# Kernel tuning notes

Measured on AMD Instinct MI355X. Metric: run time of the kernel, lower is better.

## Reference

```python
import jax, jax.numpy as jnp
import numpy as np
from jax import lax

N_SAMPLES1 = 128   # self.n_samples[0]
K = 64             # k in sample_and_group
RADIUS = 0.4       # self.radius[0]
BN_EPS = 1e-5
NEG_INF = -1e8
DIMS0 = [6, 64, 64, 128]      # mlps_in[0][0] -> mlps[0]
DIMS1 = [131, 128, 128, 512]  # 128+3 -> mlps[1] (use_light_weight=False)


def _fps(pos, n):
    # pos: (N,3) -> (n,) indices; deterministic start at point 0
    Np = pos.shape[0]
    def body(carry, _):
        dists, last = carry
        d = jnp.sum((pos - pos[last]) ** 2, axis=-1)
        dists = jnp.minimum(dists, d)
        return (dists, jnp.argmax(dists).astype(jnp.int32)), last
    _, idxs = lax.scan(body, (jnp.full((Np,), 1e10, pos.dtype), jnp.int32(0)), None, length=n)
    return idxs


def _gather(values, idx):
    # values (B,N,C), idx (B,...) -> (B,...,C)
    return jax.vmap(lambda v, i: v[i])(values, idx)


def _conv_bn_relu(x, W, b, g, be):
    # 1x1 Conv2d + BatchNorm2d (training-mode batch stats) + ReLU; x (B,n,k,Cin)
    y = jnp.einsum('bnkc,cd->bnkd', x, W) + b
    m = jnp.mean(y, axis=(0, 1, 2), keepdims=True)
    v = jnp.mean(jnp.square(y - m), axis=(0, 1, 2), keepdims=True)
    return jax.nn.relu((y - m) * lax.rsqrt(v + BN_EPS) * g + be)


def _forward(x, pos,
             W00, b00, g00, be00, W01, b01, g01, be01, W02, b02, g02, be02,
             W10, b10, g10, be10, W11, b11, g11, be11, W12, b12, g12, be12):
    # ---- stage 0: FPS + kNN grouping + conv-MLP + radius-masked max pool ----
    fidx = jax.vmap(lambda p: _fps(p, N_SAMPLES1))(pos)          # (B,128)
    sp = _gather(pos, fidx)                                      # (B,128,3) sampled_pos
    # squared pairwise distances (||a||^2+||b||^2-2ab); topk/mask on sq dist is
    # equivalent to topk/mask on sqrt dist (monotone), avoids sqrt(0) NaN grads
    sq = (jnp.sum(sp ** 2, -1)[:, :, None] + jnp.sum(pos ** 2, -1)[:, None, :]
          - 2.0 * jnp.einsum('bmd,bnd->bmn', sp, pos))           # (B,128,N)
    sq = jnp.maximum(sq, 0.0)
    neg, tidx = lax.top_k(-sq, K)                                # smallest-k
    topk_sq = -neg                                               # (B,128,64)
    gp = _gather(pos, tidx) - sp[:, :, None, :]                  # centered grouped pos
    gf = jnp.concatenate([gp, _gather(x, tidx)], axis=-1)        # (B,128,64,6)
    for (W, b, g, be) in ((W00, b00, g00, be00), (W01, b01, g01, be01), (W02, b02, g02, be02)):
        gf = _conv_bn_relu(gf, W, b, g, be)                      # (B,128,64,128)
    mask = topk_sq <= RADIUS * RADIUS
    x1 = jnp.max(jnp.where(mask[..., None], gf, NEG_INF), axis=2)  # (B,128,128)
    # ---- stage 1: global (n_samples == 1) ----
    g2 = jnp.concatenate([sp, x1], axis=-1)[:, None]             # (B,1,128,131)
    for (W, b, g, be) in ((W10, b10, g10, be10), (W11, b11, g11, be11), (W12, b12, g12, be12)):
        g2 = _conv_bn_relu(g2, W, b, g, be)                      # (B,1,128,512)
    global_x = jnp.max(g2[:, 0], axis=1, keepdims=True)          # (B,1,512)
    return global_x


def setup_inputs() -> dict:
    key = jax.random.key(0)
    ks = jax.random.split(key, 16)
    B, N = 16, 8192
    inp = {
        'x': jax.random.normal(ks[0], (B, N, 3), jnp.float32),
        'pos': jax.random.uniform(ks[1], (B, N, 3), jnp.float32),
    }
    ki = 2
    for li, dims in enumerate([DIMS0, DIMS1]):
        for ci in range(3):
            cin, cout = dims[ci], dims[ci + 1]
            inp[f'W{li}{ci}'] = jax.random.normal(ks[ki], (cin, cout), jnp.float32) * 0.05
            inp[f'b{li}{ci}'] = jnp.zeros((cout,), jnp.float32)
            inp[f'g{li}{ci}'] = jnp.ones((cout,), jnp.float32)
            inp[f'be{li}{ci}'] = jnp.zeros((cout,), jnp.float32)
            ki += 1
    return inp


def reference(x, pos,
              W00, b00, g00, be00, W01, b01, g01, be01, W02, b02, g02, be02,
              W10, b10, g10, be10, W11, b11, g11, be11, W12, b12, g12, be12):
    global_x = _forward(x, pos,
                        W00, b00, g00, be00, W01, b01, g01, be01, W02, b02, g02, be02,
                        W10, b10, g10, be10, W11, b11, g11, be11, W12, b12, g12, be12)
    pos_out = jnp.zeros((pos.shape[0], 1, 3), pos.dtype)
    return global_x, pos_out
```

## Files before the change

kernel.cpp:

```cpp
#include <hip/hip_runtime.h>
#include <cstdint>
#include <cstddef>

#define NPTS 8192
#define BATCH 16
#define MS 128
#define KNB 64
#define NBLK (BATCH * MS)

__device__ __forceinline__ float dpp_wave_max_f32(float v) {
  v = fmaxf(v, __int_as_float(__builtin_amdgcn_update_dpp((int)0xff800000, __float_as_int(v), 0x111, 0xf, 0xf, false)));
  v = fmaxf(v, __int_as_float(__builtin_amdgcn_update_dpp((int)0xff800000, __float_as_int(v), 0x112, 0xf, 0xf, false)));
  v = fmaxf(v, __int_as_float(__builtin_amdgcn_update_dpp((int)0xff800000, __float_as_int(v), 0x114, 0xf, 0xf, false)));
  v = fmaxf(v, __int_as_float(__builtin_amdgcn_update_dpp((int)0xff800000, __float_as_int(v), 0x118, 0xf, 0xf, false)));
  v = fmaxf(v, __int_as_float(__builtin_amdgcn_update_dpp((int)0xff800000, __float_as_int(v), 0x142, 0xa, 0xf, false)));
  v = fmaxf(v, __int_as_float(__builtin_amdgcn_update_dpp((int)0xff800000, __float_as_int(v), 0x143, 0xc, 0xf, false)));
  return v;
}

__device__ __forceinline__ float dpp_wave_min_f32(float v) {
  v = fminf(v, __int_as_float(__builtin_amdgcn_update_dpp(0x7f800000, __float_as_int(v), 0x111, 0xf, 0xf, false)));
  v = fminf(v, __int_as_float(__builtin_amdgcn_update_dpp(0x7f800000, __float_as_int(v), 0x112, 0xf, 0xf, false)));
  v = fminf(v, __int_as_float(__builtin_amdgcn_update_dpp(0x7f800000, __float_as_int(v), 0x114, 0xf, 0xf, false)));
  v = fminf(v, __int_as_float(__builtin_amdgcn_update_dpp(0x7f800000, __float_as_int(v), 0x118, 0xf, 0xf, false)));
  v = fminf(v, __int_as_float(__builtin_amdgcn_update_dpp(0x7f800000, __float_as_int(v), 0x142, 0xa, 0xf, false)));
  v = fminf(v, __int_as_float(__builtin_amdgcn_update_dpp(0x7f800000, __float_as_int(v), 0x143, 0xc, 0xf, false)));
  return v;
}

__device__ __forceinline__ unsigned dpp_wave_min_u32(unsigned v) {
  unsigned o;
  o = (unsigned)__builtin_amdgcn_update_dpp((int)0xffffffffu, (int)v, 0x111, 0xf, 0xf, false); v = (o < v) ? o : v;
  o = (unsigned)__builtin_amdgcn_update_dpp((int)0xffffffffu, (int)v, 0x112, 0xf, 0xf, false); v = (o < v) ? o : v;
  o = (unsigned)__builtin_amdgcn_update_dpp((int)0xffffffffu, (int)v, 0x114, 0xf, 0xf, false); v = (o < v) ? o : v;
  o = (unsigned)__builtin_amdgcn_update_dpp((int)0xffffffffu, (int)v, 0x118, 0xf, 0xf, false); v = (o < v) ? o : v;
  o = (unsigned)__builtin_amdgcn_update_dpp((int)0xffffffffu, (int)v, 0x142, 0xa, 0xf, false); v = (o < v) ? o : v;
  o = (unsigned)__builtin_amdgcn_update_dpp((int)0xffffffffu, (int)v, 0x143, 0xc, 0xf, false); v = (o < v) ? o : v;
  return v;
}

__device__ __forceinline__ float dpp_row_max_f32(float v) {
  v = fmaxf(v, __int_as_float(__builtin_amdgcn_update_dpp((int)0xff800000, __float_as_int(v), 0x111, 0xf, 0xf, false)));
  v = fmaxf(v, __int_as_float(__builtin_amdgcn_update_dpp((int)0xff800000, __float_as_int(v), 0x112, 0xf, 0xf, false)));
  v = fmaxf(v, __int_as_float(__builtin_amdgcn_update_dpp((int)0xff800000, __float_as_int(v), 0x114, 0xf, 0xf, false)));
  v = fmaxf(v, __int_as_float(__builtin_amdgcn_update_dpp((int)0xff800000, __float_as_int(v), 0x118, 0xf, 0xf, false)));
  return v;
}

__device__ __forceinline__ unsigned dpp_row_min_u32(unsigned v) {
  unsigned o;
  o = (unsigned)__builtin_amdgcn_update_dpp((int)0xffffffffu, (int)v, 0x111, 0xf, 0xf, false); v = (o < v) ? o : v;
  o = (unsigned)__builtin_amdgcn_update_dpp((int)0xffffffffu, (int)v, 0x112, 0xf, 0xf, false); v = (o < v) ? o : v;
  o = (unsigned)__builtin_amdgcn_update_dpp((int)0xffffffffu, (int)v, 0x114, 0xf, 0xf, false); v = (o < v) ? o : v;
  o = (unsigned)__builtin_amdgcn_update_dpp((int)0xffffffffu, (int)v, 0x118, 0xf, 0xf, false); v = (o < v) ? o : v;
  return v;
}

#define FPS_STEP(J)                                                        \
  {                                                                        \
    const float4 p = pts4[J * 1024 + t];                                   \
    const float dx = p.x - lx;                                             \
    const float dy = p.y - ly;                                             \
    const float dz = p.z - lz;                                             \
    const float d = dx * dx + dy * dy + dz * dz;                           \
    md##J = fminf(md##J, d);                                               \
  }

#define FPS_RESCAN(J)                                                      \
  if (md##J == wv) best = (unsigned)(J * 1024 + t);

__global__ __launch_bounds__(1024, 4) void fps_kernel(const float* __restrict__ pos,
                                                      float* __restrict__ sp) {
#pragma clang fp contract(off)
  extern __shared__ float4 pts4[];
  __shared__ float wval[2][16];
  __shared__ unsigned widx[2][16];
  const int b = blockIdx.x;
  const float* P = pos + (size_t)b * NPTS * 3;
  const int t = threadIdx.x;
  const int wave = t >> 6;
  const int lane = t & 63;
  float md0 = 1e10f, md1 = 1e10f, md2 = 1e10f, md3 = 1e10f;
  float md4 = 1e10f, md5 = 1e10f, md6 = 1e10f, md7 = 1e10f;
  for (int i = t; i < NPTS; i += 1024)
    pts4[i] = make_float4(P[i * 3 + 0], P[i * 3 + 1], P[i * 3 + 2], 0.f);
  float lx = P[0], ly = P[1], lz = P[2];
  __syncthreads();
  for (int it = 0; it < MS; ++it) {
    if (t == 0) {
      sp[((size_t)b * MS + it) * 3 + 0] = lx;
      sp[((size_t)b * MS + it) * 3 + 1] = ly;
      sp[((size_t)b * MS + it) * 3 + 2] = lz;
    }
    FPS_STEP(0) FPS_STEP(1) FPS_STEP(2) FPS_STEP(3)
    FPS_STEP(4) FPS_STEP(5) FPS_STEP(6) FPS_STEP(7)
    const float m01 = fmaxf(md0, md1), m23 = fmaxf(md2, md3);
    const float m45 = fmaxf(md4, md5), m67 = fmaxf(md6, md7);
    const float bv = fmaxf(fmaxf(m01, m23), fmaxf(m45, m67));
    const float wv = __int_as_float(
        __builtin_amdgcn_readlane(__float_as_int(dpp_wave_max_f32(bv)), 63));
    unsigned best = 0xffffffffu;
    if (bv == wv) {
      FPS_RESCAN(7) FPS_RESCAN(6) FPS_RESCAN(5) FPS_RESCAN(4)
      FPS_RESCAN(3) FPS_RESCAN(2) FPS_RESCAN(1) FPS_RESCAN(0)
    }
    const unsigned wi =
        (unsigned)__builtin_amdgcn_readlane((int)dpp_wave_min_u32(best), 63);
    const int par = it & 1;
    if (lane == 0) { wval[par][wave] = wv; widx[par][wave] = wi; }
    __syncthreads();
    const float a = wval[par][lane & 15];
    const float M = __int_as_float(
        __builtin_amdgcn_readlane(__float_as_int(dpp_row_max_f32(a)), 15));
    const unsigned c2 = (a == M) ? widx[par][lane & 15] : 0xffffffffu;
    const unsigned idx =
        (unsigned)__builtin_amdgcn_readlane((int)dpp_row_min_u32(c2), 15);
    const float4 c = pts4[idx];
    lx = c.x; ly = c.y; lz = c.z;
  }
}

__global__ __launch_bounds__(256) void knn_kernel(const float* __restrict__ pos,
                                                  const float* __restrict__ xf,
                                                  const float* __restrict__ sp,
                                                  float* __restrict__ gf0,
                                                  float* __restrict__ sqsel) {
#pragma clang fp contract(off)
  __shared__ float sqv[NPTS + 32];
  __shared__ unsigned long long wlist[4][KNB];
  __shared__ unsigned long long selk[KNB];
  const int bm = blockIdx.x;
  const int b = bm >> 7;
  const float* P = pos + (size_t)b * NPTS * 3;
  const float sx = sp[bm * 3 + 0], sy = sp[bm * 3 + 1], sz = sp[bm * 3 + 2];
  const float nsp = sx * sx + sy * sy + sz * sz;
  const int t = threadIdx.x;
  const int wave = t >> 6;
  const int lane = t & 63;
  float cv;
  unsigned ci;
  {
    unsigned long long k0 = ~0ULL;
    for (int j = 0; j < 32; ++j) {
      const int i = j * 256 + t;
      const float qx = P[i * 3 + 0], qy = P[i * 3 + 1], qz = P[i * 3 + 2];
      const float npos = qx * qx + qy * qy + qz * qz;
      const float dt = sx * qx + sy * qy + sz * qz;
      float sq = (nsp + npos) - 2.0f * dt;
      sq = fmaxf(sq, 0.0f);
      sqv[i + j] = sq;
      const unsigned long long key =
          ((unsigned long long)__float_as_uint(sq) << 32) | (unsigned)i;
      if (key < k0) k0 = key;
    }
    cv = __uint_as_float((unsigned)(k0 >> 32));
    ci = (unsigned)k0;
  }
  __syncthreads();
  unsigned cmask = 0u;
  for (int round = 0; round < KNB; ++round) {
    const float wv = __int_as_float(
        __builtin_amdgcn_readlane(__float_as_int(dpp_wave_min_f32(cv)), 63));
    const unsigned sel = (cv == wv) ? ci : 0xffffffffu;
    const unsigned wi =
        (unsigned)__builtin_amdgcn_readlane((int)dpp_wave_min_u32(sel), 63);
    if (lane == 0)
      wlist[wave][round] =
          ((unsigned long long)__float_as_uint(wv) << 32) | wi;
    const int col = (int)(wi & 255u);
    const int ownerLane = col & 63;
    const unsigned jsel = wi >> 8;
    if (lane == ownerLane) cmask |= (1u << jsel);
    const unsigned omask =
        (unsigned)__builtin_amdgcn_readlane((int)cmask, ownerLane);
    float v = __uint_as_float(0x7f800000u);
    unsigned ii = 0xffffffffu;
    if (lane < 32 && !((omask >> lane) & 1u)) {
      const int i = lane * 256 + col;
      v = sqv[i + lane];
      ii = (unsigned)i;
    }
    const float mv = __int_as_float(
        __builtin_amdgcn_readlane(__float_as_int(dpp_wave_min_f32(v)), 63));
    const unsigned s2 = (v == mv) ? ii : 0xffffffffu;
    const unsigned mi =
        (unsigned)__builtin_amdgcn_readlane((int)dpp_wave_min_u32(s2), 63);
    if (lane == ownerLane) { cv = mv; ci = mi; }
  }
  __syncthreads();
  {
    const int w = wave, r = lane;
    const unsigned long long e = wlist[w][r];
    int rank = r;
#pragma unroll
    for (int w2 = 0; w2 < 4; ++w2) {
      if (w2 == w) continue;
      int lo = 0;
#pragma unroll
      for (int step = 32; step > 0; step >>= 1)
        if (lo + step <= KNB && wlist[w2][lo + step - 1] < e) lo += step;
      rank += lo;
    }
    if (rank < KNB) selk[rank] = e;
  }
  __syncthreads();
  if (t < KNB) {
    const unsigned long long e = selk[t];
    const int i = (int)(e & 0xffffffffu);
    const float* X = xf + (size_t)b * NPTS * 3;
    const size_t base = ((size_t)bm * KNB + t) * 6;
    gf0[base + 0] = P[i * 3 + 0] - sx;
    gf0[base + 1] = P[i * 3 + 1] - sy;
    gf0[base + 2] = P[i * 3 + 2] - sz;
    gf0[base + 3] = X[i * 3 + 0];
    gf0[base + 4] = X[i * 3 + 1];
    gf0[base + 5] = X[i * 3 + 2];
    sqsel[(size_t)bm * KNB + t] = __uint_as_float((unsigned)(e >> 32));
  }
}


__global__ __launch_bounds__(256) void l1_kernel(
    const float* __restrict__ gf0, const float* __restrict__ W0,
    const float* __restrict__ B0,
    float* __restrict__ psum, float* __restrict__ psq,
    float* __restrict__ y1pre) {
  __shared__ float in6[64 * 8];
  __shared__ float wbuf[384];
  __shared__ float out[64 * 65];
  const int blk = blockIdx.x;
  const int t = threadIdx.x;
  const float* G = gf0 + (size_t)blk * 384;
  for (int i = t; i < 384; i += 256) in6[(i / 6) * 8 + (i % 6)] = G[i];
  for (int i = t; i < 384; i += 256) wbuf[i] = W0[i];
  __syncthreads();
  const int r = t >> 2;
  const int c0 = (t & 3) * 16;
  float acc[16];
#pragma unroll
  for (int j = 0; j < 16; ++j) acc[j] = B0[c0 + j];
  for (int cin = 0; cin < 6; ++cin) {
    const float a = in6[r * 8 + cin];
#pragma unroll
    for (int j = 0; j < 16; ++j) acc[j] = fmaf(a, wbuf[cin * 64 + c0 + j], acc[j]);
  }
#pragma unroll
  for (int j = 0; j < 16; ++j) out[r * 65 + c0 + j] = acc[j];
  __syncthreads();
  if (t < 64) {
    float s = 0.f, q = 0.f;
    for (int r2 = 0; r2 < 64; ++r2) { const float v = out[r2 * 65 + t]; s += v; q += v * v; }
    psum[(size_t)t * NBLK + blk] = s;
    psq[(size_t)t * NBLK + blk] = q;
  }
  float* Y = y1pre + (size_t)blk * 4096;
  for (int i = t; i < 4096; i += 256) Y[i] = out[(i >> 6) * 65 + (i & 63)];
}

__global__ __launch_bounds__(256) void l2_kernel(
    const float* __restrict__ ypre, const float* __restrict__ sc,
    const float* __restrict__ sh, const float* __restrict__ W1,
    const float* __restrict__ B1,
    float* __restrict__ psum, float* __restrict__ psq,
    float* __restrict__ yout) {
  __shared__ float As[64 * 68];
  __shared__ float Bs[64 * 64];
  __shared__ float out[64 * 68];
  const int blk = blockIdx.x;
  const int t = threadIdx.x;
  const float* Y = ypre + (size_t)blk * 4096;
  for (int i = t; i < 4096; i += 256) {
    const int c = i & 63;
    As[(i >> 6) * 68 + c] = fmaxf(fmaf(Y[i], sc[c], sh[c]), 0.f);
  }
  for (int i = t; i < 4096; i += 256) Bs[i] = W1[i];
  __syncthreads();
  const int tr = t >> 4;
  const int tc4 = (t & 15) * 4;
  float acc[4][4];
#pragma unroll
  for (int s = 0; s < 4; ++s)
#pragma unroll
    for (int j = 0; j < 4; ++j) acc[s][j] = B1[tc4 + j];
  for (int k0 = 0; k0 < 64; k0 += 4) {
    float4 av[4];
#pragma unroll
    for (int s = 0; s < 4; ++s)
      av[s] = *reinterpret_cast<const float4*>(&As[(tr + 16 * s) * 68 + k0]);
#pragma unroll
    for (int kk = 0; kk < 4; ++kk) {
      const float4 bv = *reinterpret_cast<const float4*>(&Bs[(k0 + kk) * 64 + tc4]);
#pragma unroll
      for (int s = 0; s < 4; ++s) {
        const float a = (kk == 0) ? av[s].x : (kk == 1) ? av[s].y
                       : (kk == 2) ? av[s].z : av[s].w;
        acc[s][0] = fmaf(a, bv.x, acc[s][0]);
        acc[s][1] = fmaf(a, bv.y, acc[s][1]);
        acc[s][2] = fmaf(a, bv.z, acc[s][2]);
        acc[s][3] = fmaf(a, bv.w, acc[s][3]);
      }
    }
  }
#pragma unroll
  for (int s = 0; s < 4; ++s) {
    float4 o;
    o.x = acc[s][0]; o.y = acc[s][1]; o.z = acc[s][2]; o.w = acc[s][3];
    *reinterpret_cast<float4*>(&out[(tr + 16 * s) * 68 + tc4]) = o;
  }
  __syncthreads();
  if (t < 64) {
    float s = 0.f, q = 0.f;
    for (int r2 = 0; r2 < 64; ++r2) { const float v = out[r2 * 68 + t]; s += v; q += v * v; }
    psum[(size_t)t * NBLK + blk] = s;
    psq[(size_t)t * NBLK + blk] = q;
  }
  float* O = yout + (size_t)blk * 4096;
  for (int i = t; i < 4096; i += 256) O[i] = out[(i >> 6) * 68 + (i & 63)];
}

__global__ __launch_bounds__(256) void l3_kernel(
    const float* __restrict__ ypre, const float* __restrict__ sc,
    const float* __restrict__ sh, const float* __restrict__ W2,
    const float* __restrict__ B2,
    float* __restrict__ psum, float* __restrict__ psq,
    float* __restrict__ yout) {
  __shared__ float As[64 * 68];
  __shared__ float Bs[64 * 64];
  __shared__ float out[64 * 68];
  const int blk = blockIdx.x;
  const int t = threadIdx.x;
  const float* Y = ypre + (size_t)blk * 4096;
  for (int i = t; i < 4096; i += 256) {
    const int c = i & 63;
    As[(i >> 6) * 68 + c] = fmaxf(fmaf(Y[i], sc[c], sh[c]), 0.f);
  }
  const int tr = t >> 4;
  const int tc4 = (t & 15) * 4;
  for (int hc = 0; hc < 2; ++hc) {
    __syncthreads();
    for (int i = t; i < 4096; i += 256)
      Bs[i] = W2[(i >> 6) * 128 + hc * 64 + (i & 63)];
    __syncthreads();
    float acc[4][4];
#pragma unroll
    for (int s = 0; s < 4; ++s)
#pragma unroll
      for (int j = 0; j < 4; ++j) acc[s][j] = B2[hc * 64 + tc4 + j];
    for (int k0 = 0; k0 < 64; k0 += 4) {
      float4 av[4];
#pragma unroll
      for (int s = 0; s < 4; ++s)
        av[s] = *reinterpret_cast<const float4*>(&As[(tr + 16 * s) * 68 + k0]);
#pragma unroll
      for (int kk = 0; kk < 4; ++kk) {
        const float4 bv = *reinterpret_cast<const float4*>(&Bs[(k0 + kk) * 64 + tc4]);
#pragma unroll
        for (int s = 0; s < 4; ++s) {
          const float a = (kk == 0) ? av[s].x : (kk == 1) ? av[s].y
                         : (kk == 2) ? av[s].z : av[s].w;
          acc[s][0] = fmaf(a, bv.x, acc[s][0]);
          acc[s][1] = fmaf(a, bv.y, acc[s][1]);
          acc[s][2] = fmaf(a, bv.z, acc[s][2]);
          acc[s][3] = fmaf(a, bv.w, acc[s][3]);
        }
      }
    }
#pragma unroll
    for (int s = 0; s < 4; ++s) {
      float4 o;
      o.x = acc[s][0]; o.y = acc[s][1]; o.z = acc[s][2]; o.w = acc[s][3];
      *reinterpret_cast<float4*>(&out[(tr + 16 * s) * 68 + tc4]) = o;
    }
    __syncthreads();
    if (t < 64) {
      float s = 0.f, q = 0.f;
      for (int r2 = 0; r2 < 64; ++r2) { const float v = out[r2 * 68 + t]; s += v; q += v * v; }
      psum[(size_t)(hc * 64 + t) * NBLK + blk] = s;
      psq[(size_t)(hc * 64 + t) * NBLK + blk] = q;
    }
    float* O = yout + (size_t)blk * 8192;
    for (int i = t; i < 4096; i += 256)
      O[(i >> 6) * 128 + hc * 64 + (i & 63)] = out[(i >> 6) * 68 + (i & 63)];
  }
}

__global__ __launch_bounds__(128) void l4_kernel(
    const float* __restrict__ y3pre, const float* __restrict__ sc3,
    const float* __restrict__ sh3, const float* __restrict__ sqsel,
    float* __restrict__ x1) {
  __shared__ float sqs[64];
  const int blk = blockIdx.x;
  const int t = threadIdx.x;
  if (t < 64) sqs[t] = sqsel[(size_t)blk * 64 + t];
  __syncthreads();
  const float scv = sc3[t], shv = sh3[t];
  const float* Y = y3pre + (size_t)blk * 8192;
  float mx = -1e8f;
  for (int r = 0; r < 64; ++r) {
    const float act = fmaxf(fmaf(Y[r * 128 + t], scv, shv), 0.f);
    const float v = (sqs[r] <= 0.16f) ? act : -1e8f;
    mx = fmaxf(mx, v);
  }
  x1[(size_t)blk * 128 + t] = mx;
}

__global__ __launch_bounds__(256) void p_stats(const float* __restrict__ psum,
                                               const float* __restrict__ psq,
                                               float invN,
                                               const float* __restrict__ g,
                                               const float* __restrict__ be,
                                               float* __restrict__ sc,
                                               float* __restrict__ sh) {
  const int c = blockIdx.x;
  const int t = threadIdx.x;
  double s = 0.0, q = 0.0;
  for (int k = t; k < NBLK; k += 256) {
    s += (double)psum[(size_t)c * NBLK + k];
    q += (double)psq[(size_t)c * NBLK + k];
  }
  __shared__ double ss[256], qq[256];
  ss[t] = s;
  qq[t] = q;
  __syncthreads();
  for (int st = 128; st > 0; st >>= 1) {
    if (t < st) { ss[t] += ss[t + st]; qq[t] += qq[t + st]; }
    __syncthreads();
  }
  if (t == 0) {
    const double mean = ss[0] * (double)invN;
    double var = qq[0] * (double)invN - mean * mean;
    if (var < 0.0) var = 0.0;
    const float scl = (float)((double)g[c] / sqrt(var + 1e-5));
    sc[c] = scl;
    sh[c] = be[c] - (float)mean * scl;
  }
}

__global__ __launch_bounds__(128) void s1_kernel(const float* __restrict__ sp,
                                                 const float* __restrict__ x1,
                                                 const float* __restrict__ W,
                                                 const float* __restrict__ bia,
                                                 float* __restrict__ y1) {
  __shared__ float row[132];
  const int rowid = blockIdx.x;
  const int t = threadIdx.x;
  if (t < 3) row[t] = sp[(size_t)rowid * 3 + t];
  row[3 + t] = x1[(size_t)rowid * 128 + t];
  __syncthreads();
  float acc = bia[t];
  for (int cin = 0; cin < 131; ++cin) acc = fmaf(row[cin], W[(size_t)cin * 128 + t], acc);
  y1[(size_t)rowid * 128 + t] = acc;
}

__global__ __launch_bounds__(128) void s2_kernel(const float* __restrict__ y1,
                                                 const float* __restrict__ sc, const float* __restrict__ sh,
                                                 const float* __restrict__ W, const float* __restrict__ bia,
                                                 float* __restrict__ y2) {
  __shared__ float row[128];
  const int rowid = blockIdx.x;
  const int t = threadIdx.x;
  row[t] = fmaxf(fmaf(y1[(size_t)rowid * 128 + t], sc[t], sh[t]), 0.f);
  __syncthreads();
  float acc = bia[t];
  for (int cin = 0; cin < 128; ++cin) acc = fmaf(row[cin], W[(size_t)cin * 128 + t], acc);
  y2[(size_t)rowid * 128 + t] = acc;
}

__global__ __launch_bounds__(256) void s3_kernel(const float* __restrict__ y2,
                                                 const float* __restrict__ sc, const float* __restrict__ sh,
                                                 const float* __restrict__ W, const float* __restrict__ bia,
                                                 float* __restrict__ y3) {
  __shared__ float row[128];
  const int rowid = blockIdx.x;
  const int t = threadIdx.x;
  if (t < 128) row[t] = fmaxf(fmaf(y2[(size_t)rowid * 128 + t], sc[t], sh[t]), 0.f);
  __syncthreads();
  for (int h = 0; h < 2; ++h) {
    const int c = h * 256 + t;
    float acc = bia[c];
    for (int cin = 0; cin < 128; ++cin) acc = fmaf(row[cin], W[(size_t)cin * 512 + c], acc);
    y3[(size_t)rowid * 512 + c] = acc;
  }
}

__global__ __launch_bounds__(256) void s_stats(const float* __restrict__ y, int C, int rows,
                                               const float* __restrict__ g, const float* __restrict__ be,
                                               float* __restrict__ sc, float* __restrict__ sh) {
  const int c = blockIdx.x;
  const int t = threadIdx.x;
  double s = 0.0, q = 0.0;
  for (int r2 = t; r2 < rows; r2 += 256) {
    const double v = (double)y[(size_t)r2 * C + c];
    s += v;
    q += v * v;
  }
  __shared__ double ss[256], qq[256];
  ss[t] = s;
  qq[t] = q;
  __syncthreads();
  for (int st = 128; st > 0; st >>= 1) {
    if (t < st) { ss[t] += ss[t + st]; qq[t] += qq[t + st]; }
    __syncthreads();
  }
  if (t == 0) {
    const double mean = ss[0] / rows;
    double var = qq[0] / rows - mean * mean;
    if (var < 0.0) var = 0.0;
    const float scl = (float)((double)g[c] / sqrt(var + 1e-5));
    sc[c] = scl;
    sh[c] = be[c] - (float)mean * scl;
  }
}

__global__ __launch_bounds__(256) void final_kernel(const float* __restrict__ y3,
                                                    const float* __restrict__ sc, const float* __restrict__ sh,
                                                    float* __restrict__ out) {
  const int gid = blockIdx.x * 256 + threadIdx.x;
  const int b = gid >> 9;
  const int c = gid & 511;
  const float scv = sc[c], shv = sh[c];
  float mx = -3.402823466e+38f;
  for (int m = 0; m < 128; ++m) {
    const float v = fmaxf(fmaf(y3[((size_t)(b * 128 + m)) * 512 + c], scv, shv), 0.f);
    mx = fmaxf(mx, v);
  }
  out[gid] = mx;
  if (gid < 48) out[8192 + gid] = 0.f;
}

extern "C" void kernel_launch(void* const* d_in, const int* in_sizes, int n_in,
                              void* d_out, int out_size, void* d_ws, size_t ws_size,
                              hipStream_t stream) {
  const float* x    = (const float*)d_in[0];
  const float* pos  = (const float*)d_in[1];
  const float* W00  = (const float*)d_in[2];
  const float* b00  = (const float*)d_in[3];
  const float* g00  = (const float*)d_in[4];
  const float* be00 = (const float*)d_in[5];
  const float* W01  = (const float*)d_in[6];
  const float* b01  = (const float*)d_in[7];
  const float* g01  = (const float*)d_in[8];
  const float* be01 = (const float*)d_in[9];
  const float* W02  = (const float*)d_in[10];
  const float* b02  = (const float*)d_in[11];
  const float* g02  = (const float*)d_in[12];
  const float* be02 = (const float*)d_in[13];
  const float* W10  = (const float*)d_in[14];
  const float* b10  = (const float*)d_in[15];
  const float* g10  = (const float*)d_in[16];
  const float* be10 = (const float*)d_in[17];
  const float* W11  = (const float*)d_in[18];
  const float* b11  = (const float*)d_in[19];
  const float* g11  = (const float*)d_in[20];
  const float* be11 = (const float*)d_in[21];
  const float* W12  = (const float*)d_in[22];
  const float* b12  = (const float*)d_in[23];
  const float* g12  = (const float*)d_in[24];
  const float* be12 = (const float*)d_in[25];

  float* w = (float*)d_ws;
  float* sp    = w;
  float* gf0   = sp + 6144;
  float* sqsel = gf0 + 786432;
  float* x1    = sqsel + 131072;
  float* parts = x1 + 262144;
  float* psum  = parts;
  float* psq   = parts + 128 * NBLK;
  float* st    = parts + 524288;
  float* sc1 = st + 0,    *sh1 = st + 64;
  float* sc2 = st + 128,  *sh2 = st + 192;
  float* sc3 = st + 256,  *sh3 = st + 384;
  float* t1sc = st + 512, *t1sh = st + 640;
  float* t2sc = st + 768, *t2sh = st + 896;
  float* t3sc = st + 1024, *t3sh = st + 1536;
  float* y1s = st + 2048;
  float* y2s = y1s + 262144;
  float* y3s = y2s + 262144;
  const size_t BASE = 3284992;
  float* y1pre = w + BASE;
  float* y2pre = y1pre + 8388608;
  float* y3pre = y2pre + 8388608;
  const size_t NEED = BASE + 8388608ULL * 2 + 16777216ULL;
  (void)NEED;

  fps_kernel<<<BATCH, 1024, NPTS * sizeof(float4), stream>>>(pos, sp);
  knn_kernel<<<BATCH * MS, 256, 0, stream>>>(pos, x, sp, gf0, sqsel);

  const float invN0 = 1.0f / (float)(NBLK * KNB);
  l1_kernel<<<NBLK, 256, 0, stream>>>(gf0, W00, b00, psum, psq, y1pre);
  p_stats<<<64, 256, 0, stream>>>(psum, psq, invN0, g00, be00, sc1, sh1);
  l2_kernel<<<NBLK, 256, 0, stream>>>(y1pre, sc1, sh1, W01, b01, psum, psq, y2pre);
  p_stats<<<64, 256, 0, stream>>>(psum, psq, invN0, g01, be01, sc2, sh2);
  l3_kernel<<<NBLK, 256, 0, stream>>>(y2pre, sc2, sh2, W02, b02, psum, psq, y3pre);
  p_stats<<<128, 256, 0, stream>>>(psum, psq, invN0, g02, be02, sc3, sh3);
  l4_kernel<<<NBLK, 128, 0, stream>>>(y3pre, sc3, sh3, sqsel, x1);

  s1_kernel<<<NBLK, 128, 0, stream>>>(sp, x1, W10, b10, y1s);
  s_stats<<<128, 256, 0, stream>>>(y1s, 128, NBLK, g10, be10, t1sc, t1sh);
  s2_kernel<<<NBLK, 128, 0, stream>>>(y1s, t1sc, t1sh, W11, b11, y2s);
  s_stats<<<128, 256, 0, stream>>>(y2s, 128, NBLK, g11, be11, t2sc, t2sh);
  s3_kernel<<<NBLK, 256, 0, stream>>>(y2s, t2sc, t2sh, W12, b12, y3s);
  s_stats<<<512, 256, 0, stream>>>(y3s, 512, NBLK, g12, be12, t3sc, t3sh);
  final_kernel<<<32, 256, 0, stream>>>(y3s, t3sc, t3sh, (float*)d_out);
}
```

Measured before the change: 432.2 us.

## Split FPS into two launches and fuse l4+s1 and stats+final kernels

The FPS kernel now runs in two launches of 64 iterations each, saving per-thread min-distance state and the last point to workspace between them. The l4 max-pool kernel is fused with the s1 matvec, and the last BN-stats kernel is fused with the final max-pool, which removes an intermediate buffer and two launches. Splitting FPS adds a launch plus a reload of the point cloud into shared memory, and the FPS loop itself still runs on only 16 blocks.

```diff
diff --git a/kernel.cpp b/kernel.cpp
--- a/kernel.cpp
+++ b/kernel.cpp
@@ -70,7 +70,10 @@
   if (md##J == wv) best = (unsigned)(J * 1024 + t);
 
 __global__ __launch_bounds__(1024, 4) void fps_kernel(const float* __restrict__ pos,
-                                                      float* __restrict__ sp) {
+                                                      float* __restrict__ sp,
+                                                      float* __restrict__ mdst,
+                                                      float* __restrict__ lastst,
+                                                      int it0) {
 #pragma clang fp contract(off)
   extern __shared__ float4 pts4[];
   __shared__ float wval[2][16];
@@ -80,13 +83,23 @@
   const int t = threadIdx.x;
   const int wave = t >> 6;
   const int lane = t & 63;
-  float md0 = 1e10f, md1 = 1e10f, md2 = 1e10f, md3 = 1e10f;
-  float md4 = 1e10f, md5 = 1e10f, md6 = 1e10f, md7 = 1e10f;
+  float md0, md1, md2, md3, md4, md5, md6, md7;
   for (int i = t; i < NPTS; i += 1024)
     pts4[i] = make_float4(P[i * 3 + 0], P[i * 3 + 1], P[i * 3 + 2], 0.f);
-  float lx = P[0], ly = P[1], lz = P[2];
-  __syncthreads();
-  for (int it = 0; it < MS; ++it) {
+  float lx, ly, lz;
+  float* M = mdst + ((size_t)b * 1024 + t) * 8;
+  if (it0 == 0) {
+    md0 = md1 = md2 = md3 = md4 = md5 = md6 = md7 = 1e10f;
+    lx = P[0]; ly = P[1]; lz = P[2];
+  } else {
+    const float4 a = *reinterpret_cast<const float4*>(M);
+    const float4 c = *reinterpret_cast<const float4*>(M + 4);
+    md0 = a.x; md1 = a.y; md2 = a.z; md3 = a.w;
+    md4 = c.x; md5 = c.y; md6 = c.z; md7 = c.w;
+    lx = lastst[b * 4 + 0]; ly = lastst[b * 4 + 1]; lz = lastst[b * 4 + 2];
+  }
+  __syncthreads();
+  for (int it = it0; it < it0 + MS / 2; ++it) {
     if (t == 0) {
       sp[((size_t)b * MS + it) * 3 + 0] = lx;
       sp[((size_t)b * MS + it) * 3 + 1] = ly;
@@ -110,13 +123,25 @@
     if (lane == 0) { wval[par][wave] = wv; widx[par][wave] = wi; }
     __syncthreads();
     const float a = wval[par][lane & 15];
-    const float M = __int_as_float(
+    const float Mx = __int_as_float(
         __builtin_amdgcn_readlane(__float_as_int(dpp_row_max_f32(a)), 15));
-    const unsigned c2 = (a == M) ? widx[par][lane & 15] : 0xffffffffu;
+    const unsigned c2 = (a == Mx) ? widx[par][lane & 15] : 0xffffffffu;
     const unsigned idx =
         (unsigned)__builtin_amdgcn_readlane((int)dpp_row_min_u32(c2), 15);
     const float4 c = pts4[idx];
     lx = c.x; ly = c.y; lz = c.z;
+  }
+  {
+    float4 a, c;
+    a.x = md0; a.y = md1; a.z = md2; a.w = md3;
+    c.x = md4; c.y = md5; c.z = md6; c.w = md7;
+    *reinterpret_cast<float4*>(M) = a;
+    *reinterpret_cast<float4*>(M + 4) = c;
+    if (t == 0) {
+      lastst[b * 4 + 0] = lx;
+      lastst[b * 4 + 1] = ly;
+      lastst[b * 4 + 2] = lz;
+    }
   }
 }
 
@@ -219,7 +244,6 @@
   }
 }
 
-
 __global__ __launch_bounds__(256) void l1_kernel(
     const float* __restrict__ gf0, const float* __restrict__ W0,
     const float* __restrict__ B0,
@@ -384,11 +408,13 @@
   }
 }
 
-__global__ __launch_bounds__(128) void l4_kernel(
+__global__ __launch_bounds__(128) void l4s1_kernel(
     const float* __restrict__ y3pre, const float* __restrict__ sc3,
     const float* __restrict__ sh3, const float* __restrict__ sqsel,
-    float* __restrict__ x1) {
+    const float* __restrict__ sp, const float* __restrict__ W,
+    const float* __restrict__ bia, float* __restrict__ y1) {
   __shared__ float sqs[64];
+  __shared__ float row[132];
   const int blk = blockIdx.x;
   const int t = threadIdx.x;
   if (t < 64) sqs[t] = sqsel[(size_t)blk * 64 + t];
@@ -401,7 +427,12 @@
     const float v = (sqs[r] <= 0.16f) ? act : -1e8f;
     mx = fmaxf(mx, v);
   }
-  x1[(size_t)blk * 128 + t] = mx;
+  if (t < 3) row[t] = sp[(size_t)blk * 3 + t];
+  row[3 + t] = mx;
+  __syncthreads();
+  float acc = bia[t];
+  for (int cin = 0; cin < 131; ++cin) acc = fmaf(row[cin], W[(size_t)cin * 128 + t], acc);
+  y1[(size_t)blk * 128 + t] = acc;
 }
 
 __global__ __launch_bounds__(256) void p_stats(const float* __restrict__ psum,
@@ -436,22 +467,6 @@
   }
 }
 
-__global__ __launch_bounds__(128) void s1_kernel(const float* __restrict__ sp,
-                                                 const float* __restrict__ x1,
-                                                 const float* __restrict__ W,
-                                                 const float* __restrict__ bia,
-                                                 float* __restrict__ y1) {
-  __shared__ float row[132];
-  const int rowid = blockIdx.x;
-  const int t = threadIdx.x;
-  if (t < 3) row[t] = sp[(size_t)rowid * 3 + t];
-  row[3 + t] = x1[(size_t)rowid * 128 + t];
-  __syncthreads();
-  float acc = bia[t];
-  for (int cin = 0; cin < 131; ++cin) acc = fmaf(row[cin], W[(size_t)cin * 128 + t], acc);
-  y1[(size_t)rowid * 128 + t] = acc;
-}
-
 __global__ __launch_bounds__(128) void s2_kernel(const float* __restrict__ y1,
                                                  const float* __restrict__ sc, const float* __restrict__ sh,
                                                  const float* __restrict__ W, const float* __restrict__ bia,
@@ -512,20 +527,52 @@
   }
 }
 
-__global__ __launch_bounds__(256) void final_kernel(const float* __restrict__ y3,
-                                                    const float* __restrict__ sc, const float* __restrict__ sh,
-                                                    float* __restrict__ out) {
-  const int gid = blockIdx.x * 256 + threadIdx.x;
-  const int b = gid >> 9;
-  const int c = gid & 511;
-  const float scv = sc[c], shv = sh[c];
+__global__ __launch_bounds__(256) void s_stats_final(const float* __restrict__ y3,
+                                                     const float* __restrict__ g,
+                                                     const float* __restrict__ be,
+                                                     float* __restrict__ out) {
+  const int c = blockIdx.x;
+  const int t = threadIdx.x;
+  double s = 0.0, q = 0.0;
+  for (int r2 = t; r2 < NBLK; r2 += 256) {
+    const double v = (double)y3[(size_t)r2 * 512 + c];
+    s += v;
+    q += v * v;
+  }
+  __shared__ double ss[256], qq[256];
+  __shared__ float sscl, sshv;
+  ss[t] = s;
+  qq[t] = q;
+  __syncthreads();
+  for (int st = 128; st > 0; st >>= 1) {
+    if (t < st) { ss[t] += ss[t + st]; qq[t] += qq[t + st]; }
+    __syncthreads();
+  }
+  if (t == 0) {
+    const double mean = ss[0] / NBLK;
+    double var = qq[0] / NBLK - mean * mean;
+    if (var < 0.0) var = 0.0;
+    const float scl = (float)((double)g[c] / sqrt(var + 1e-5));
+    sscl = scl;
+    sshv = be[c] - (float)mean * scl;
+  }
+  __syncthreads();
+  const float scl = sscl, shv = sshv;
   float mx = -3.402823466e+38f;
-  for (int m = 0; m < 128; ++m) {
-    const float v = fmaxf(fmaf(y3[((size_t)(b * 128 + m)) * 512 + c], scv, shv), 0.f);
+  for (int k = 0; k < 8; ++k) {
+    const int r = t * 8 + k;
+    const float v = fmaxf(fmaf(y3[(size_t)r * 512 + c], scl, shv), 0.f);
     mx = fmaxf(mx, v);
   }
-  out[gid] = mx;
-  if (gid < 48) out[8192 + gid] = 0.f;
+  __shared__ float pmax[256];
+  pmax[t] = mx;
+  __syncthreads();
+  if (t < 16) {
+    float m = -3.402823466e+38f;
+    for (int j = 0; j < 16; ++j) m = fmaxf(m, pmax[t * 16 + j]);
+    out[(size_t)t * 512 + c] = m;
+  }
+  if (c == 0 && t < 48) out[8192 + t] = 0.f;
 }
 
 extern "C" void kernel_launch(void* const* d_in, const int* in_sizes, int n_in,
@@ -572,7 +619,6 @@
   float* sc3 = st + 256,  *sh3 = st + 384;
   float* t1sc = st + 512, *t1sh = st + 640;
   float* t2sc = st + 768, *t2sh = st + 896;
-  float* t3sc = st + 1024, *t3sh = st + 1536;
   float* y1s = st + 2048;
   float* y2s = y1s + 262144;
   float* y3s = y2s + 262144;
@@ -580,10 +626,11 @@
   float* y1pre = w + BASE;
   float* y2pre = y1pre + 8388608;
   float* y3pre = y2pre + 8388608;
-  const size_t NEED = BASE + 8388608ULL * 2 + 16777216ULL;
-  (void)NEED;
-
-  fps_kernel<<<BATCH, 1024, NPTS * sizeof(float4), stream>>>(pos, sp);
+  float* mdws  = y3pre + 16777216;
+  float* lastw = mdws + 131072;
+
+  fps_kernel<<<BATCH, 1024, NPTS * sizeof(float4), stream>>>(pos, sp, mdws, lastw, 0);
+  fps_kernel<<<BATCH, 1024, NPTS * sizeof(float4), stream>>>(pos, sp, mdws, lastw, 64);
   knn_kernel<<<BATCH * MS, 256, 0, stream>>>(pos, x, sp, gf0, sqsel);
 
   const float invN0 = 1.0f / (float)(NBLK * KNB);
@@ -593,13 +640,11 @@
   p_stats<<<64, 256, 0, stream>>>(psum, psq, invN0, g01, be01, sc2, sh2);
   l3_kernel<<<NBLK, 256, 0, stream>>>(y2pre, sc2, sh2, W02, b02, psum, psq, y3pre);
   p_stats<<<128, 256, 0, stream>>>(psum, psq, invN0, g02, be02, sc3, sh3);
-  l4_kernel<<<NBLK, 128, 0, stream>>>(y3pre, sc3, sh3, sqsel, x1);
-
-  s1_kernel<<<NBLK, 128, 0, stream>>>(sp, x1, W10, b10, y1s);
+  l4s1_kernel<<<NBLK, 128, 0, stream>>>(y3pre, sc3, sh3, sqsel, sp, W10, b10, y1s);
+
   s_stats<<<128, 256, 0, stream>>>(y1s, 128, NBLK, g10, be10, t1sc, t1sh);
   s2_kernel<<<NBLK, 128, 0, stream>>>(y1s, t1sc, t1sh, W11, b11, y2s);
   s_stats<<<128, 256, 0, stream>>>(y2s, 128, NBLK, g11, be11, t2sc, t2sh);
   s3_kernel<<<NBLK, 256, 0, stream>>>(y2s, t2sc, t2sh, W12, b12, y3s);
-  s_stats<<<512, 256, 0, stream>>>(y3s, 512, NBLK, g12, be12, t3sc, t3sh);
-  final_kernel<<<32, 256, 0, stream>>>(y3s, t3sc, t3sh, (float*)d_out);
-}
+  s_stats_final<<<512, 256, 0, stream>>>(y3s, g12, be12, (float*)d_out);
+}
```

Result: no change. 433.8 us (+0.4%).
